# Performance work log

Measured on AMD Instinct MI355X. Metric: run time of the kernel, lower is better.

The kernel has to match this reference:

```python
import jax, jax.numpy as jnp
import numpy as np

SPEC_WINDOW = 64
SPEC_HOP = 32
PELT_PENALTY = 5.0
PATCH_MIN = 8
PATCH_MAX = 64
PATCH_GRID = 2
ANCHOR_LEN = 16
GEN_ALPHA = 1.0
GEN_BETA = 1.0
REGIME_DIM = 3

# ---------------- host-side (numpy) data-dependent segmentation ----------------

def _segment_stats(seg):
    # dominant period + normalized spectral bandwidth of a 1D segment
    n = int(seg.shape[0])
    if n < 4:
        return float(max(n, 1)), 0.0
    s = seg - seg.mean()
    spec = np.abs(np.fft.rfft(s)) ** 2
    tail = spec[1:]
    tot = float(tail.sum())
    if tot <= 0.0:
        return float(n), 0.0
    k = int(np.argmax(tail)) + 1
    dom_period = n / k
    p = tail / tot
    nf = tail.shape[0]
    f = np.arange(1, nf + 1, dtype=np.float64) / nf
    c = float((p * f).sum())
    bw = float(np.sqrt((p * (f - c) ** 2).sum()))
    return float(dom_period), bw


def _patch_length(dom_period, bw):
    raw = GEN_ALPHA * dom_period / (1.0 + GEN_BETA * bw)
    pl = int(PATCH_GRID * round(raw / PATCH_GRID))
    return int(min(max(pl, PATCH_MIN), PATCH_MAX))


def _detect_boundaries(sig):
    # local spectral features over sliding windows + PELT (L2 cost) changepoints
    L = int(sig.shape[0])
    if L <= max(2, PATCH_MIN) or L < SPEC_WINDOW:
        return [0, L]
    starts = np.arange(0, L - SPEC_WINDOW + 1, SPEC_HOP)
    frames = sig[starts[:, None] + np.arange(SPEC_WINDOW)]
    frames = frames - frames.mean(axis=1, keepdims=True)
    spec = np.abs(np.fft.rfft(frames * np.hanning(SPEC_WINDOW)[None, :], axis=1)) ** 2
    feats = np.log(spec + 1e-8)  # [n_windows, F]
    n, d = feats.shape
    cs = np.concatenate([np.zeros((1, d)), np.cumsum(feats, 0)], 0)
    cs2 = np.concatenate([np.zeros((1, d)), np.cumsum(feats ** 2, 0)], 0)
    Fc = np.full(n + 1, np.inf)
    Fc[0] = -PELT_PENALTY
    prev = np.zeros(n + 1, dtype=np.int64)
    cands = np.array([0], dtype=np.int64)
    for t in range(1, n + 1):
        nn = (t - cands).astype(np.float64)
        ssum = cs[t] - cs[cands]
        ssum2 = cs2[t] - cs2[cands]
        cost = (ssum2 - ssum ** 2 / nn[:, None]).sum(axis=1)
        vals = Fc[cands] + cost + PELT_PENALTY
        i = int(np.argmin(vals))
        Fc[t] = vals[i]
        prev[t] = cands[i]
        cands = np.concatenate([cands[vals <= Fc[t] + PELT_PENALTY], [t]])
    bps = []
    t = n
    while t > 0:
        bps.append(int(t))
        t = int(prev[t])
    bps = sorted(bps)
    bounds = [0]
    for k in bps[:-1]:
        b = int(starts[k]) if k < len(starts) else L
        b = min(b, L)
        if b - bounds[-1] >= PATCH_MIN:
            bounds.append(b)
    if L - bounds[-1] < PATCH_MIN and len(bounds) > 1:
        bounds.pop()
    bounds.append(L)
    return bounds


def _build_plan(sig):
    L = int(sig.shape[0])
    if L <= 0:
        return [(0, 0, 1, 1.0, 0.0)]
    bounds = _detect_boundaries(sig)
    plan = []
    for s, e in zip(bounds[:-1], bounds[1:]):
        if e <= s:
            continue
        dp, bw = _segment_stats(sig[s:e])
        plan.append((int(s), int(e), _patch_length(dp, bw), float(dp), float(bw)))
    if not plan:
        dp, bw = _segment_stats(sig)
        plan = [(0, L, _patch_length(dp, bw), float(dp), float(bw))]
    return plan

# ---------------- jnp ops ----------------

def _resize_linear(x, out_len):
    # matches F.interpolate(mode='linear', align_corners=False) along last axis
    in_len = x.shape[-1]
    if in_len == out_len:
        return x
    scale = in_len / out_len
    coords = (jnp.arange(out_len, dtype=jnp.float32) + 0.5) * scale - 0.5
    coords = jnp.clip(coords, 0.0, in_len - 1)
    lo = jnp.floor(coords).astype(jnp.int32)
    hi = jnp.minimum(lo + 1, in_len - 1)
    w = (coords - lo).astype(x.dtype)
    return x[..., lo] * (1 - w) + x[..., hi] * w


def setup_inputs() -> dict:
    key = jax.random.key(0)
    x = jax.random.normal(key, (32, 32, 16384), dtype=jnp.float32)
    return {"x": x}


def reference(x):
    B, C, L = x.shape
    x_np = np.asarray(x)
    plans = [_build_plan(x_np[b].mean(axis=0).astype(np.float32)) for b in range(B)]
    denom_c = float(max(L - 1, 1))
    denom_s = float(max(L, 1))

    per = []
    max_tok = 0
    for b in range(B):
        series = x[b]
        pch, sch, ech, rch = [], [], [], []
        for (s, e, pl, dp, bw) in plans[b]:
            if e <= s:
                continue
            seg_len = e - s
            regime = np.array([dp / denom_s, bw, seg_len / denom_s], dtype=np.float32)
            n_full = seg_len // pl
            full_len = n_full * pl
            if n_full > 0:
                full = jnp.transpose(series[:, s:s + full_len].reshape(C, n_full, pl), (1, 0, 2))
                pch.append(_resize_linear(full, ANCHOR_LEN))
                st = s + np.arange(n_full, dtype=np.int64) * pl
                sch.append(st)
                ech.append(st + pl)
                rch.append(np.broadcast_to(regime, (n_full, REGIME_DIM)).copy())
            if full_len < seg_len:
                pch.append(_resize_linear(series[:, s + full_len:e], ANCHOR_LEN)[None])
                sch.append(np.array([s + full_len], dtype=np.int64))
                ech.append(np.array([e], dtype=np.int64))
                rch.append(regime[None])
        patches = jnp.concatenate(pch, axis=0)
        per.append((patches, np.concatenate(sch), np.concatenate(ech), np.concatenate(rch)))
        max_tok = max(max_tok, patches.shape[0])

    pouts = []
    mask = np.zeros((B, max_tok), dtype=bool)
    start_out = np.zeros((B, max_tok), dtype=np.int32)
    end_out = np.zeros((B, max_tok), dtype=np.int32)
    center_out = np.zeros((B, max_tok, 1), dtype=np.float32)
    span_out = np.zeros((B, max_tok, 1), dtype=np.float32)
    regime_out = np.zeros((B, max_tok, REGIME_DIM), dtype=np.float32)
    n_tok = np.zeros((B,), dtype=np.int32)
    for b, (p, st, en, rg) in enumerate(per):
        n = p.shape[0]
        pouts.append(jnp.concatenate([p, jnp.zeros((max_tok - n, C, ANCHOR_LEN), x.dtype)], 0))
        mask[b, :n] = True
        start_out[b, :n] = st
        end_out[b, :n] = en
        center_out[b, :n, 0] = (st.astype(np.float32) + en.astype(np.float32) - 1.0) * 0.5 / denom_c
        span_out[b, :n, 0] = (en - st).astype(np.float32) / denom_s
        regime_out[b, :n] = rg
        n_tok[b] = n
    patches_out = jnp.stack(pouts, 0)
    return (patches_out, jnp.asarray(mask), jnp.asarray(start_out), jnp.asarray(end_out),
            jnp.asarray(center_out), jnp.asarray(span_out), jnp.asarray(regime_out), jnp.asarray(n_tok))
```

## Files before the change

### kernel.cpp

```cpp
#include <hip/hip_runtime.h>
#include <math.h>

#define Bn 32
#define Cn 32
#define Ln 16384
#define NF 511
#define NB 33
#define MAXSEG 512
#define TB 8192
#define PEN 5.0

__global__ void k_sig(const float* __restrict__ x, float* __restrict__ sig) {
    int idx = blockIdx.x * 256 + threadIdx.x;
    if (idx >= Bn * Ln) return;
    int b = idx >> 14;
    int t = idx & (Ln - 1);
    const float* p = x + ((size_t)b * Cn) * Ln + t;
    float a = p[0];
    #pragma unroll
    for (int c = 1; c < Cn; c++) a += p[(size_t)c * Ln];
    sig[idx] = a / 32.0f;
}

__global__ void k_fmean(const float* __restrict__ sig, float* __restrict__ fm) {
    int idx = blockIdx.x * 256 + threadIdx.x;
    if (idx >= Bn * NF) return;
    int b = idx / NF, f = idx - b * NF;
    const float* a = sig + b * Ln + f * 32;
    float r[8];
    #pragma unroll
    for (int j = 0; j < 8; j++) r[j] = a[j];
    #pragma unroll
    for (int base = 8; base < 64; base += 8)
        #pragma unroll
        for (int j = 0; j < 8; j++) r[j] += a[base + j];
    float res = ((r[0] + r[1]) + (r[2] + r[3])) + ((r[4] + r[5]) + (r[6] + r[7]));
    fm[idx] = res / 64.0f;
}

__global__ void k_feats(const float* __restrict__ sig, const float* __restrict__ fm,
                        double* __restrict__ feats) {
    __shared__ double v[64], ct[64], stb[64];
    int bf = blockIdx.x;
    int b = bf / NF, f = bf - b * NF;
    int i = threadIdx.x;
    double ang = (2.0 * M_PI * (double)i) / 64.0;
    double sn, cx;
    sincos(ang, &sn, &cx);
    ct[i] = cx; stb[i] = sn;
    int n2 = 2 * i - 63;
    double w = 0.5 + 0.5 * cos((M_PI * (double)n2) / 63.0);
    float m = fm[bf];
    v[i] = (double)(sig[b * Ln + f * 32 + i] - m) * w;
    __syncthreads();
    if (i < NB) {
        double re = 0.0, im = 0.0;
        for (int t = 0; t < 64; t++) {
            int j = (t * i) & 63;
            re += v[t] * ct[j];
            im += v[t] * stb[j];
        }
        double spec = re * re + im * im;
        feats[(size_t)bf * NB + i] = log(spec + 1e-8);
    }
}

__global__ void k_cumsum(const double* __restrict__ feats, double* __restrict__ cs,
                         double* __restrict__ cs2) {
    int idx = blockIdx.x * 256 + threadIdx.x;
    if (idx >= Bn * NB) return;
    int b = idx / NB, d = idx - b * NB;
    const double* fp = feats + (size_t)b * NF * NB + d;
    double* c1 = cs + (size_t)b * 512 * NB + d;
    double* c2 = cs2 + (size_t)b * 512 * NB + d;
    double a1 = 0.0, a2 = 0.0;
    c1[0] = 0.0; c2[0] = 0.0;
    for (int t = 0; t < NF; t++) {
        double vv = fp[(size_t)t * NB];
        a1 += vv;
        a2 += vv * vv;
        c1[(size_t)(t + 1) * NB] = a1;
        c2[(size_t)(t + 1) * NB] = a2;
    }
}

__global__ __launch_bounds__(256) void k_cost(const double* __restrict__ cs,
                                              const double* __restrict__ cs2,
                                              double* __restrict__ costM) {
    int z = blockIdx.x;
    int b = blockIdx.y;
    const double* c1 = cs + (size_t)b * 512 * NB;
    const double* c2 = cs2 + (size_t)b * 512 * NB;
    for (int t = z + 1; t <= NF; t += 32) {
        const double* ct1 = c1 + (size_t)t * NB;
        const double* ct2 = c2 + (size_t)t * NB;
        double* outp = costM + ((size_t)b * 512 + (size_t)t) * 512;
        for (int c = threadIdx.x; c < t; c += 256) {
            double nn = (double)(t - c);
            const double* p1 = c1 + (size_t)c * NB;
            const double* p2 = c2 + (size_t)c * NB;
            double r[8];
            #pragma unroll
            for (int j = 0; j < 8; j++) {
                double ss = ct1[j] - p1[j]; double s2 = ct2[j] - p2[j];
                r[j] = s2 - ss * ss / nn;
            }
            #pragma unroll
            for (int base = 8; base < 32; base += 8)
                #pragma unroll
                for (int j = 0; j < 8; j++) {
                    int d = base + j;
                    double ss = ct1[d] - p1[d]; double s2 = ct2[d] - p2[d];
                    r[j] += s2 - ss * ss / nn;
                }
            double res = ((r[0] + r[1]) + (r[2] + r[3])) + ((r[4] + r[5]) + (r[6] + r[7]));
            { double ss = ct1[32] - p1[32]; double s2 = ct2[32] - p2[32]; res += s2 - ss * ss / nn; }
            outp[c] = res;
        }
    }
}

template <int CTRL>
__device__ __forceinline__ double dpp_mov_f64(double v) {
    int lo = __double2loint(v), hi = __double2hiint(v);
    int slo = __builtin_amdgcn_update_dpp(lo, lo, CTRL, 0xF, 0xF, false);
    int shi = __builtin_amdgcn_update_dpp(hi, hi, CTRL, 0xF, 0xF, false);
    return __hiloint2double(shi, slo);
}
__device__ __forceinline__ double rl_f64(double v, int l) {
    int lo = __builtin_amdgcn_readlane(__double2loint(v), l);
    int hi = __builtin_amdgcn_readlane(__double2hiint(v), l);
    return __hiloint2double(hi, lo);
}
__device__ __forceinline__ double wave_min_f64(double v) {
    v = fmin(v, dpp_mov_f64<0x111>(v));
    v = fmin(v, dpp_mov_f64<0x112>(v));
    v = fmin(v, dpp_mov_f64<0x114>(v));
    v = fmin(v, dpp_mov_f64<0x118>(v));
    double a = rl_f64(v, 15), b = rl_f64(v, 31);
    double c = rl_f64(v, 47), d = rl_f64(v, 63);
    return fmin(fmin(a, b), fmin(c, d));
}

template <int NP>
__device__ __forceinline__ void pelt_step(int t, int lane, const double (&cur)[8],
                                          double (&fcreg)[8], int* __restrict__ prevOut) {
    double vals[NP];
    #pragma unroll
    for (int p = 0; p < NP; p++) vals[p] = fcreg[p] + cur[p] + PEN;
    double red[NP];
    #pragma unroll
    for (int p = 0; p < NP; p++) red[p] = vals[p];
    #pragma unroll
    for (int s = 1; s < NP; s <<= 1)
        #pragma unroll
        for (int p = 0; p + s < NP; p += 2 * s) red[p] = fmin(red[p], red[p + s]);
    double bmin = wave_min_f64(red[0]);
    int bc = 0;
    #pragma unroll
    for (int p = NP - 1; p >= 0; p--) {
        unsigned long long m = __ballot(vals[p] == bmin);
        if (m != 0ull) bc = (p << 6) + (__ffsll(m) - 1);
    }
    if (lane == 0) prevOut[t] = bc;
    double thr = bmin + PEN;
    #pragma unroll
    for (int p = 0; p < NP; p++)
        if (!(vals[p] <= thr)) fcreg[p] = INFINITY;
    #pragma unroll
    for (int p = NP - 1; p <= NP; p++)
        if (p < 8 && p == (t >> 6) && lane == (t & 63)) fcreg[p] = bmin;
}

template <int K>
__device__ __forceinline__ void pelt_phase(const double* __restrict__ cm, int lane,
                                           double (&fcreg)[8], int* __restrict__ prevOut) {
    constexpr int NP = K + 1;
    const int t0 = 64 * K + 1;
    const int t1 = (64 * K + 64 < NF) ? (64 * K + 64) : NF;
    double r0[8], r1[8], n0[8], n1[8];
    #pragma unroll
    for (int p = 0; p < NP; p++) {
        r0[p] = cm[(size_t)t0 * 512 + (p << 6) + lane];
        r1[p] = cm[(size_t)(t0 + 1) * 512 + (p << 6) + lane];
    }
    int t = t0;
    for (; t + 1 <= t1; t += 2) {
        int q0 = t + 2, q1 = t + 3;
        if (q0 > NF) q0 = NF;
        if (q1 > NF) q1 = NF;
        #pragma unroll
        for (int p = 0; p < NP; p++) {
            n0[p] = cm[(size_t)q0 * 512 + (p << 6) + lane];
            n1[p] = cm[(size_t)q1 * 512 + (p << 6) + lane];
        }
        pelt_step<NP>(t, lane, r0, fcreg, prevOut);
        pelt_step<NP>(t + 1, lane, r1, fcreg, prevOut);
        #pragma unroll
        for (int p = 0; p < NP; p++) { r0[p] = n0[p]; r1[p] = n1[p]; }
    }
    if (t <= t1) pelt_step<NP>(t, lane, r0, fcreg, prevOut);
}

__global__ __launch_bounds__(64, 1) void k_pelt(const double* __restrict__ costM,
                                                int* __restrict__ prevG) {
    int b = blockIdx.x;
    int lane = threadIdx.x;
    const double* cm = costM + (size_t)b * 512 * 512;
    int* prevOut = prevG + b * 512;
    double fcreg[8];
    #pragma unroll
    for (int p = 0; p < 8; p++) fcreg[p] = INFINITY;
    if (lane == 0) fcreg[0] = -PEN;
    pelt_phase<0>(cm, lane, fcreg, prevOut);
    pelt_phase<1>(cm, lane, fcreg, prevOut);
    pelt_phase<2>(cm, lane, fcreg, prevOut);
    pelt_phase<3>(cm, lane, fcreg, prevOut);
    pelt_phase<4>(cm, lane, fcreg, prevOut);
    pelt_phase<5>(cm, lane, fcreg, prevOut);
    pelt_phase<6>(cm, lane, fcreg, prevOut);
    pelt_phase<7>(cm, lane, fcreg, prevOut);
}

__global__ __launch_bounds__(64) void k_pelt_slow(const double* __restrict__ cs,
                                                  const double* __restrict__ cs2,
                                                  int* __restrict__ prevG) {
    __shared__ double sFc[512];
    __shared__ double sVal[512];
    __shared__ unsigned short sCand[512];
    int b = blockIdx.x;
    int lane = threadIdx.x;
    const double* c1 = cs + (size_t)b * 512 * NB;
    const double* c2 = cs2 + (size_t)b * 512 * NB;
    if (lane == 0) { sFc[0] = -PEN; sCand[0] = 0; }
    __syncthreads();
    int ncand = 1;
    for (int t = 1; t <= NF; t++) {
        const double* ct1 = c1 + (size_t)t * NB;
        const double* ct2 = c2 + (size_t)t * NB;
        int passes = (ncand + 63) >> 6;
        double bmv = INFINITY;
        int bmi = 0x7fffffff;
        for (int p = 0; p < passes; p++) {
            int slot = (p << 6) + lane;
            double val = INFINITY;
            if (slot < ncand) {
                int cc = sCand[slot];
                double nn = (double)(t - cc);
                const double* p1 = c1 + (size_t)cc * NB;
                const double* p2 = c2 + (size_t)cc * NB;
                double r[8];
                #pragma unroll
                for (int j = 0; j < 8; j++) {
                    double ss = ct1[j] - p1[j]; double s2 = ct2[j] - p2[j];
                    r[j] = s2 - ss * ss / nn;
                }
                #pragma unroll
                for (int base = 8; base < 32; base += 8)
                    #pragma unroll
                    for (int j = 0; j < 8; j++) {
                        int d = base + j;
                        double ss = ct1[d] - p1[d]; double s2 = ct2[d] - p2[d];
                        r[j] += s2 - ss * ss / nn;
                    }
                double res = ((r[0] + r[1]) + (r[2] + r[3])) + ((r[4] + r[5]) + (r[6] + r[7]));
                { double ss = ct1[32] - p1[32]; double s2 = ct2[32] - p2[32]; res += s2 - ss * ss / nn; }
                val = sFc[cc] + res + PEN;
                if (val < bmv) { bmv = val; bmi = slot; }
            }
            sVal[slot] = val;
        }
        #pragma unroll
        for (int off = 1; off < 64; off <<= 1) {
            double ov = __shfl_xor(bmv, off);
            int oi = __shfl_xor(bmi, off);
            if (ov < bmv || (ov == bmv && oi < bmi)) { bmv = ov; bmi = oi; }
        }
        double thr = bmv + PEN;
        if (lane == 0) {
            sFc[t] = bmv;
            prevG[b * 512 + t] = (int)sCand[bmi];
        }
        __syncthreads();
        int base = 0;
        for (int p = 0; p < passes; p++) {
            int slot = (p << 6) + lane;
            int cc = (slot < ncand) ? (int)sCand[slot] : 0;
            bool keep = (slot < ncand) && (sVal[slot] <= thr);
            unsigned long long mask = __ballot(keep);
            if (keep) sCand[base + __popcll(mask & ((1ull << lane) - 1ull))] = (unsigned short)cc;
            base += (int)__popcll(mask);
        }
        if (lane == 0) sCand[base] = (unsigned short)t;
        ncand = base + 1;
        __syncthreads();
    }
}

__global__ __launch_bounds__(64) void k_bounds(const int* __restrict__ prevG,
                                               int* __restrict__ segS, int* __restrict__ segE,
                                               int* __restrict__ nsegA, int* __restrict__ binoff) {
    __shared__ int sPrev[512];
    __shared__ int sBp[512];
    __shared__ int sBd[520];
    __shared__ int sNs;
    int b = blockIdx.x;
    int tid = threadIdx.x;
    const int* pv = prevG + b * 512;
    #pragma unroll
    for (int i = 0; i < 8; i++) sPrev[tid + i * 64] = pv[tid + i * 64];
    __syncthreads();
    if (tid == 0) {
        int cnt = 0, t = NF;
        while (t > 0) { sBp[cnt++] = t; t = sPrev[t]; }
        int nbv = 1; sBd[0] = 0; int last = 0;
        for (int i = cnt - 1; i >= 1; --i) {
            int k = sBp[i];
            int bb = 32 * k;
            if (bb > Ln) bb = Ln;
            if (bb - last >= 8) { sBd[nbv++] = bb; last = bb; }
        }
        if (Ln - last < 8 && nbv > 1) nbv--;
        sBd[nbv++] = Ln;
        int ns = nbv - 1;
        nsegA[b] = ns;
        sNs = ns;
    }
    __syncthreads();
    int ns = sNs;
    for (int j = tid; j < ns; j += 64) {
        int s = sBd[j], e = sBd[j + 1];
        segS[b * 512 + j] = s;
        segE[b * 512 + j] = e;
        binoff[b * 513 + j] = s >> 1;
    }
    if (tid == 0) binoff[b * 513 + ns] = sBd[ns] >> 1;
}

__global__ void k_segmean(const float* __restrict__ sig, const int* __restrict__ segS,
                          const int* __restrict__ segE, const int* __restrict__ nsegA,
                          double* __restrict__ segMean) {
    __shared__ double red[256];
    int b = blockIdx.y, j = blockIdx.x;
    if (j >= nsegA[b]) return;
    int s = segS[b * 512 + j], e = segE[b * 512 + j];
    double acc = 0.0;
    for (int i = s + threadIdx.x; i < e; i += 256) acc += (double)sig[b * Ln + i];
    red[threadIdx.x] = acc;
    __syncthreads();
    for (int st = 128; st >= 1; st >>= 1) {
        if (threadIdx.x < st) red[threadIdx.x] += red[threadIdx.x + st];
        __syncthreads();
    }
    if (threadIdx.x == 0) segMean[b * 512 + j] = red[0] / (double)(e - s);
}

__global__ __launch_bounds__(256) void k_spec(const float* __restrict__ sig,
                                              const double* __restrict__ segMean,
                                              const int* __restrict__ segS, const int* __restrict__ segE,
                                              const int* __restrict__ nsegA, const int* __restrict__ binoff,
                                              double* __restrict__ spec) {
    int b = blockIdx.y;
    int wv = threadIdx.x >> 6, lane = threadIdx.x & 63;
    int slot = blockIdx.x * 4 + wv;
    int ns = nsegA[b];
    const int* off = binoff + b * 513;
    if (slot >= off[ns]) return;
    int lo = 0, hi = ns - 1;
    while (lo < hi) { int mid = (lo + hi + 1) >> 1; if (off[mid] <= slot) lo = mid; else hi = mid - 1; }
    int j = lo;
    int s = segS[b * 512 + j], e = segE[b * 512 + j], n = e - s;
    int k = slot - off[j] + 1;
    float m32 = (float)segMean[b * 512 + j];
    long j0 = ((long)lane * (long)k) % (long)n;
    long js = (64L * (long)k) % (long)n;
    double a0 = (2.0 * M_PI * (double)j0) / (double)n;
    double as = (2.0 * M_PI * (double)js) / (double)n;
    double cr, sr, cb, sb;
    sincos(a0, &sr, &cr);
    sincos(as, &sb, &cb);
    double re = 0.0, im = 0.0;
    const float* sp = sig + b * Ln + s;
    for (int tt = lane; tt < n; tt += 64) {
        double v = (double)(sp[tt] - m32);
        re += v * cr;
        im += v * sr;
        double nc = cr * cb - sr * sb;
        sr = sr * cb + cr * sb;
        cr = nc;
    }
    #pragma unroll
    for (int o = 32; o >= 1; o >>= 1) { re += __shfl_down(re, o); im += __shfl_down(im, o); }
    if (lane == 0) spec[(size_t)b * TB + slot] = re * re + im * im;
}

__global__ void k_stats(const double* __restrict__ spec, const int* __restrict__ segS,
                        const int* __restrict__ segE, const int* __restrict__ nsegA,
                        const int* __restrict__ binoff, int* __restrict__ segPL,
                        double* __restrict__ segDP, double* __restrict__ segBW,
                        int* __restrict__ segNT) {
    __shared__ double rv[256]; __shared__ int ri[256];
    __shared__ double rt[256], rs[256];
    __shared__ double sC, sTot;
    int b = blockIdx.y, j = blockIdx.x;
    if (j >= nsegA[b]) return;
    int s = segS[b * 512 + j], e = segE[b * 512 + j], n = e - s, nf = n >> 1;
    const double* base = spec + (size_t)b * TB + binoff[b * 513 + j];
    int tid = threadIdx.x;
    double mv = -INFINITY; int mi = 0x7fffffff; double tot = 0.0, s1 = 0.0;
    for (int i = tid; i < nf; i += 256) {
        double vv = base[i];
        double f = (double)(i + 1) / (double)nf;
        tot += vv; s1 += vv * f;
        if (vv > mv) { mv = vv; mi = i; }
    }
    rv[tid] = mv; ri[tid] = mi; rt[tid] = tot; rs[tid] = s1;
    __syncthreads();
    for (int st = 128; st >= 1; st >>= 1) {
        if (tid < st) {
            double ov = rv[tid + st]; int oi = ri[tid + st];
            if (ov > rv[tid] || (ov == rv[tid] && oi < ri[tid])) { rv[tid] = ov; ri[tid] = oi; }
            rt[tid] += rt[tid + st]; rs[tid] += rs[tid + st];
        }
        __syncthreads();
    }
    if (tid == 0) { sTot = rt[0]; sC = rs[0] / rt[0]; }
    __syncthreads();
    double c = sC, totv = sTot;
    double s2 = 0.0;
    for (int i = tid; i < nf; i += 256) {
        double f = (double)(i + 1) / (double)nf;
        double d = f - c;
        s2 += base[i] * d * d;
    }
    rt[tid] = s2;
    __syncthreads();
    for (int st = 128; st >= 1; st >>= 1) {
        if (tid < st) rt[tid] += rt[tid + st];
        __syncthreads();
    }
    if (tid == 0) {
        double dp, bw;
        if (n < 4) { dp = (double)(n > 0 ? n : 1); bw = 0.0; }
        else if (!(totv > 0.0)) { dp = (double)n; bw = 0.0; }
        else { int kk = ri[0] + 1; dp = (double)n / (double)kk; bw = sqrt(rt[0] / totv); }
        double raw = 1.0 * dp / (1.0 + 1.0 * bw);
        double rr = rint(raw / 2.0);
        long pl = 2L * (long)rr;
        if (pl < 8) pl = 8;
        if (pl > 64) pl = 64;
        int nfull = n / (int)pl;
        int ntok = nfull + ((nfull * (int)pl < n) ? 1 : 0);
        segPL[b * 512 + j] = (int)pl; segDP[b * 512 + j] = dp;
        segBW[b * 512 + j] = bw; segNT[b * 512 + j] = ntok;
    }
}

__global__ __launch_bounds__(64) void k_tokpref(const int* __restrict__ nsegA,
                                                const int* __restrict__ segNT,
                                                int* __restrict__ tokoff, int* __restrict__ ntokA) {
    __shared__ int sNT[512];
    __shared__ int sOff[513];
    int b = blockIdx.x, tid = threadIdx.x;
    int ns = nsegA[b];
    for (int j = tid; j < ns; j += 64) sNT[j] = segNT[b * 512 + j];
    __syncthreads();
    if (tid == 0) {
        int off = 0;
        for (int j = 0; j < ns; j++) { sOff[j] = off; off += sNT[j]; }
        sOff[ns] = off;
        ntokA[b] = off;
    }
    __syncthreads();
    for (int j = tid; j <= ns; j += 64) tokoff[b * 513 + j] = sOff[j];
}

__global__ __launch_bounds__(256) void k_fill(const float* __restrict__ x,
                                              const int* __restrict__ segS, const int* __restrict__ segE,
                                              const int* __restrict__ segPL, const double* __restrict__ segDP,
                                              const double* __restrict__ segBW, const int* __restrict__ nsegA,
                                              const int* __restrict__ tokoff, const int* __restrict__ ntokA,
                                              float* __restrict__ out, int MT) {
    int b = blockIdx.y, tok = blockIdx.x;
    int nt = ntokA[b];
    if (tok >= nt) return;
    int ns = nsegA[b];
    const int* toff = tokoff + b * 513;
    int lo = 0, hi = ns - 1;
    while (lo < hi) { int mid = (lo + hi + 1) >> 1; if (toff[mid] <= tok) lo = mid; else hi = mid - 1; }
    int j = lo;
    int s = segS[b * 512 + j], e = segE[b * 512 + j], pl = segPL[b * 512 + j];
    int idx = tok - toff[j];
    int nfull = (e - s) / pl;
    int st, en;
    if (idx < nfull) { st = s + idx * pl; en = st + pl; }
    else { st = s + nfull * pl; en = e; }
    int ilen = en - st;
    float scale = (float)ilen / 16.0f;
    int tid = threadIdx.x;
    size_t pbase = ((size_t)(b * MT + tok)) * (Cn * 16);
    const float* xb = x + (size_t)b * Cn * Ln;
    #pragma unroll
    for (int r = 0; r < 2; r++) {
        int eidx = tid + r * 256;
        int c = eidx >> 4, jo = eidx & 15;
        float coords = ((float)jo + 0.5f) * scale - 0.5f;
        if (coords < 0.0f) coords = 0.0f;
        float mx = (float)(ilen - 1);
        if (coords > mx) coords = mx;
        int l2 = (int)floorf(coords);
        int h2 = l2 + 1;
        if (h2 > ilen - 1) h2 = ilen - 1;
        float w = coords - (float)l2;
        const float* xc = xb + (size_t)c * Ln + st;
        out[pbase + eidx] = xc[l2] * (1.0f - w) + xc[h2] * w;
    }
    if (tid == 0) {
        size_t BT = (size_t)Bn * MT;
        size_t o_mask = BT * 512;
        size_t pos = (size_t)b * MT + tok;
        out[o_mask + pos] = 1.0f;
        out[o_mask + BT + pos] = (float)st;
        out[o_mask + 2 * BT + pos] = (float)en;
        out[o_mask + 3 * BT + pos] = (((float)st + (float)en) - 1.0f) * 0.5f / 16383.0f;
        out[o_mask + 4 * BT + pos] = (float)(en - st) / 16384.0f;
        double dp = segDP[b * 512 + j], bwv = segBW[b * 512 + j];
        size_t o_rg = o_mask + 5 * BT;
        out[o_rg + pos * 3 + 0] = (float)(dp / 16384.0);
        out[o_rg + pos * 3 + 1] = (float)bwv;
        out[o_rg + pos * 3 + 2] = (float)((double)(e - s) / 16384.0);
        if (tok == 0) out[o_mask + 8 * BT + b] = (float)nt;
    }
}

extern "C" void kernel_launch(void* const* d_in, const int* in_sizes, int n_in,
                              void* d_out, int out_size, void* d_ws, size_t ws_size,
                              hipStream_t stream) {
    (void)in_sizes; (void)n_in;
    const float* x = (const float*)d_in[0];
    float* out = (float*)d_out;
    char* ws = (char*)d_ws;
    size_t o = 0;
    auto alloc = [&](size_t bytes) -> char* {
        char* r = ws + o;
        o = (o + bytes + 511) & ~(size_t)511;
        return r;
    };
    float* sig = (float*)alloc((size_t)Bn * Ln * 4);
    float* fm = (float*)alloc((size_t)Bn * NF * 4);
    double* feats = (double*)alloc((size_t)Bn * NF * NB * 8);
    double* cs = (double*)alloc((size_t)Bn * 512 * NB * 8);
    double* cs2 = (double*)alloc((size_t)Bn * 512 * NB * 8);
    int* prevG = (int*)alloc((size_t)Bn * 512 * 4);
    int* nsegA = (int*)alloc((size_t)Bn * 4);
    int* segS = (int*)alloc((size_t)Bn * 512 * 4);
    int* segE = (int*)alloc((size_t)Bn * 512 * 4);
    int* segPL = (int*)alloc((size_t)Bn * 512 * 4);
    int* segNT = (int*)alloc((size_t)Bn * 512 * 4);
    double* segDP = (double*)alloc((size_t)Bn * 512 * 8);
    double* segBW = (double*)alloc((size_t)Bn * 512 * 8);
    double* segMean = (double*)alloc((size_t)Bn * 512 * 8);
    int* binoff = (int*)alloc((size_t)Bn * 513 * 4);
    int* tokoff = (int*)alloc((size_t)Bn * 513 * 4);
    int* ntokA = (int*)alloc((size_t)Bn * 4);
    double* spec = (double*)alloc((size_t)Bn * TB * 8);
    size_t costBytes = (size_t)Bn * 512 * 512 * 8;
    double* costM = (double*)alloc(costBytes);
    bool haveCost = (o <= ws_size);

    int MT = (out_size / Bn - 1) / 520;

    hipMemsetAsync(d_out, 0, (size_t)out_size * 4, stream);
    k_sig<<<(Bn * Ln + 255) / 256, 256, 0, stream>>>(x, sig);
    k_fmean<<<(Bn * NF + 255) / 256, 256, 0, stream>>>(sig, fm);
    k_feats<<<Bn * NF, 64, 0, stream>>>(sig, fm, feats);
    k_cumsum<<<(Bn * NB + 255) / 256, 256, 0, stream>>>(feats, cs, cs2);
    if (haveCost) {
        k_cost<<<dim3(32, Bn), 256, 0, stream>>>(cs, cs2, costM);
        k_pelt<<<Bn, 64, 0, stream>>>(costM, prevG);
    } else {
        k_pelt_slow<<<Bn, 64, 0, stream>>>(cs, cs2, prevG);
    }
    k_bounds<<<Bn, 64, 0, stream>>>(prevG, segS, segE, nsegA, binoff);
    k_segmean<<<dim3(MAXSEG, Bn), 256, 0, stream>>>(sig, segS, segE, nsegA, segMean);
    k_spec<<<dim3(TB / 4, Bn), 256, 0, stream>>>(sig, segMean, segS, segE, nsegA, binoff, spec);
    k_stats<<<dim3(MAXSEG, Bn), 256, 0, stream>>>(spec, segS, segE, nsegA, binoff,
                                                  segPL, segDP, segBW, segNT);
    k_tokpref<<<Bn, 64, 0, stream>>>(nsegA, segNT, tokoff, ntokA);
    if (MT > 0)
        k_fill<<<dim3(MT, Bn), 256, 0, stream>>>(x, segS, segE, segPL, segDP, segBW,
                                                 nsegA, tokoff, ntokA, out, MT);
}
```

Before: 1.066 ms.

## Transpose cumsum layout and block cost matrix over four rows per pass

The cumulative sums are stored feature-major ([b][d][t]), so threads reading consecutive candidate indices c get coalesced loads. The cost kernel now handles four t rows per pass, staging their prefix sums in shared memory and reusing each c column load across four outputs. Rows are paired front and back (4g+1 and 508-4g) so each of the 64 blocks gets a balanced share of the triangle. The serial cumsum now writes with a stride between threads, and the fallback PELT path reads with strided gathers, so those two kernels may get slower.

```diff
diff --git a/kernel.cpp b/kernel.cpp
--- a/kernel.cpp
+++ b/kernel.cpp
@@ -65,57 +65,116 @@
     }
 }
 
-__global__ void k_cumsum(const double* __restrict__ feats, double* __restrict__ cs,
-                         double* __restrict__ cs2) {
+__global__ void k_cumsum(const double* __restrict__ feats, double* __restrict__ csT,
+                         double* __restrict__ cs2T) {
     int idx = blockIdx.x * 256 + threadIdx.x;
     if (idx >= Bn * NB) return;
     int b = idx / NB, d = idx - b * NB;
     const double* fp = feats + (size_t)b * NF * NB + d;
-    double* c1 = cs + (size_t)b * 512 * NB + d;
-    double* c2 = cs2 + (size_t)b * 512 * NB + d;
+    double* c1 = csT + ((size_t)b * NB + d) * 512;
+    double* c2 = cs2T + ((size_t)b * NB + d) * 512;
     double a1 = 0.0, a2 = 0.0;
     c1[0] = 0.0; c2[0] = 0.0;
     for (int t = 0; t < NF; t++) {
         double vv = fp[(size_t)t * NB];
         a1 += vv;
         a2 += vv * vv;
-        c1[(size_t)(t + 1) * NB] = a1;
-        c2[(size_t)(t + 1) * NB] = a2;
-    }
-}
-
-__global__ __launch_bounds__(256) void k_cost(const double* __restrict__ cs,
-                                              const double* __restrict__ cs2,
+        c1[t + 1] = a1;
+        c2[t + 1] = a2;
+    }
+}
+
+__global__ __launch_bounds__(256) void k_cost(const double* __restrict__ csT,
+                                              const double* __restrict__ cs2T,
                                               double* __restrict__ costM) {
-    int z = blockIdx.x;
+    __shared__ double s1[4][NB], s2s[4][NB];
+    int g = blockIdx.x;
     int b = blockIdx.y;
-    const double* c1 = cs + (size_t)b * 512 * NB;
-    const double* c2 = cs2 + (size_t)b * 512 * NB;
-    for (int t = z + 1; t <= NF; t += 32) {
-        const double* ct1 = c1 + (size_t)t * NB;
-        const double* ct2 = c2 + (size_t)t * NB;
-        double* outp = costM + ((size_t)b * 512 + (size_t)t) * 512;
-        for (int c = threadIdx.x; c < t; c += 256) {
-            double nn = (double)(t - c);
-            const double* p1 = c1 + (size_t)c * NB;
-            const double* p2 = c2 + (size_t)c * NB;
-            double r[8];
+    const double* c1 = csT + (size_t)b * NB * 512;
+    const double* c2 = cs2T + (size_t)b * NB * 512;
+    double* outb = costM + (size_t)b * 512 * 512;
+
+    for (int ph = 0; ph < 2; ph++) {
+        int tbase = (ph == 0) ? (4 * g + 1) : (508 - 4 * g);
+        __syncthreads();
+        for (int i = threadIdx.x; i < 4 * NB; i += 256) {
+            int ti = i / NB, j = i - ti * NB;
+            s1[ti][j]  = c1[(size_t)j * 512 + (tbase + ti)];
+            s2s[ti][j] = c2[(size_t)j * 512 + (tbase + ti)];
+        }
+        __syncthreads();
+        int t0 = tbase, t3 = tbase + 3;
+
+        for (int c = threadIdx.x; c < t0; c += 256) {
+            double nn0 = (double)(tbase     - c);
+            double nn1 = (double)(tbase + 1 - c);
+            double nn2 = (double)(tbase + 2 - c);
+            double nn3 = (double)(tbase + 3 - c);
+            double rA[8], rB[8], rC[8], rD[8];
             #pragma unroll
             for (int j = 0; j < 8; j++) {
-                double ss = ct1[j] - p1[j]; double s2 = ct2[j] - p2[j];
-                r[j] = s2 - ss * ss / nn;
+                double a1 = c1[(size_t)j * 512 + c];
+                double a2 = c2[(size_t)j * 512 + c];
+                { double ss = s1[0][j] - a1, sv = s2s[0][j] - a2; rA[j] = sv - ss * ss / nn0; }
+                { double ss = s1[1][j] - a1, sv = s2s[1][j] - a2; rB[j] = sv - ss * ss / nn1; }
+                { double ss = s1[2][j] - a1, sv = s2s[2][j] - a2; rC[j] = sv - ss * ss / nn2; }
+                { double ss = s1[3][j] - a1, sv = s2s[3][j] - a2; rD[j] = sv - ss * ss / nn3; }
             }
-            #pragma unroll
-            for (int base = 8; base < 32; base += 8)
+            for (int base = 8; base < 32; base += 8) {
                 #pragma unroll
                 for (int j = 0; j < 8; j++) {
                     int d = base + j;
-                    double ss = ct1[d] - p1[d]; double s2 = ct2[d] - p2[d];
-                    r[j] += s2 - ss * ss / nn;
+                    double a1 = c1[(size_t)d * 512 + c];
+                    double a2 = c2[(size_t)d * 512 + c];
+                    { double ss = s1[0][d] - a1, sv = s2s[0][d] - a2; rA[j] += sv - ss * ss / nn0; }
+                    { double ss = s1[1][d] - a1, sv = s2s[1][d] - a2; rB[j] += sv - ss * ss / nn1; }
+                    { double ss = s1[2][d] - a1, sv = s2s[2][d] - a2; rC[j] += sv - ss * ss / nn2; }
+                    { double ss = s1[3][d] - a1, sv = s2s[3][d] - a2; rD[j] += sv - ss * ss / nn3; }
                 }
-            double res = ((r[0] + r[1]) + (r[2] + r[3])) + ((r[4] + r[5]) + (r[6] + r[7]));
-            { double ss = ct1[32] - p1[32]; double s2 = ct2[32] - p2[32]; res += s2 - ss * ss / nn; }
-            outp[c] = res;
+            }
+            double a1 = c1[(size_t)32 * 512 + c];
+            double a2 = c2[(size_t)32 * 512 + c];
+            double res0 = ((rA[0] + rA[1]) + (rA[2] + rA[3])) + ((rA[4] + rA[5]) + (rA[6] + rA[7]));
+            double res1 = ((rB[0] + rB[1]) + (rB[2] + rB[3])) + ((rB[4] + rB[5]) + (rB[6] + rB[7]));
+            double res2 = ((rC[0] + rC[1]) + (rC[2] + rC[3])) + ((rC[4] + rC[5]) + (rC[6] + rC[7]));
+            double res3 = ((rD[0] + rD[1]) + (rD[2] + rD[3])) + ((rD[4] + rD[5]) + (rD[6] + rD[7]));
+            { double ss = s1[0][32] - a1, sv = s2s[0][32] - a2; res0 += sv - ss * ss / nn0; }
+            { double ss = s1[1][32] - a1, sv = s2s[1][32] - a2; res1 += sv - ss * ss / nn1; }
+            { double ss = s1[2][32] - a1, sv = s2s[2][32] - a2; res2 += sv - ss * ss / nn2; }
+            { double ss = s1[3][32] - a1, sv = s2s[3][32] - a2; res3 += sv - ss * ss / nn3; }
+            outb[(size_t)(tbase    ) * 512 + c] = res0;
+            outb[(size_t)(tbase + 1) * 512 + c] = res1;
+            outb[(size_t)(tbase + 2) * 512 + c] = res2;
+            outb[(size_t)(tbase + 3) * 512 + c] = res3;
+        }
+
+        for (int c = t0 + threadIdx.x; c < t3; c += 256) {
+            for (int ti = 0; ti < 4; ti++) {
+                int t = tbase + ti;
+                if (c >= t) continue;
+                double nn = (double)(t - c);
+                double r[8];
+                #pragma unroll
+                for (int j = 0; j < 8; j++) {
+                    double ss = s1[ti][j] - c1[(size_t)j * 512 + c];
+                    double sv = s2s[ti][j] - c2[(size_t)j * 512 + c];
+                    r[j] = sv - ss * ss / nn;
+                }
+                for (int base = 8; base < 32; base += 8) {
+                    #pragma unroll
+                    for (int j = 0; j < 8; j++) {
+                        int d = base + j;
+                        double ss = s1[ti][d] - c1[(size_t)d * 512 + c];
+                        double sv = s2s[ti][d] - c2[(size_t)d * 512 + c];
+                        r[j] += sv - ss * ss / nn;
+                    }
+                }
+                double res = ((r[0] + r[1]) + (r[2] + r[3])) + ((r[4] + r[5]) + (r[6] + r[7]));
+                { double ss = s1[ti][32] - c1[(size_t)32 * 512 + c];
+                  double sv = s2s[ti][32] - c2[(size_t)32 * 512 + c];
+                  res += sv - ss * ss / nn; }
+                outb[(size_t)t * 512 + c] = res;
+            }
         }
     }
 }
@@ -222,22 +281,20 @@
     pelt_phase<7>(cm, lane, fcreg, prevOut);
 }
 
-__global__ __launch_bounds__(64) void k_pelt_slow(const double* __restrict__ cs,
-                                                  const double* __restrict__ cs2,
+__global__ __launch_bounds__(64) void k_pelt_slow(const double* __restrict__ csT,
+                                                  const double* __restrict__ cs2T,
                                                   int* __restrict__ prevG) {
     __shared__ double sFc[512];
     __shared__ double sVal[512];
     __shared__ unsigned short sCand[512];
     int b = blockIdx.x;
     int lane = threadIdx.x;
-    const double* c1 = cs + (size_t)b * 512 * NB;
-    const double* c2 = cs2 + (size_t)b * 512 * NB;
+    const double* c1 = csT + (size_t)b * NB * 512;
+    const double* c2 = cs2T + (size_t)b * NB * 512;
     if (lane == 0) { sFc[0] = -PEN; sCand[0] = 0; }
     __syncthreads();
     int ncand = 1;
     for (int t = 1; t <= NF; t++) {
-        const double* ct1 = c1 + (size_t)t * NB;
-        const double* ct2 = c2 + (size_t)t * NB;
         int passes = (ncand + 63) >> 6;
         double bmv = INFINITY;
         int bmi = 0x7fffffff;
@@ -247,12 +304,11 @@
             if (slot < ncand) {
                 int cc = sCand[slot];
                 double nn = (double)(t - cc);
-                const double* p1 = c1 + (size_t)cc * NB;
-                const double* p2 = c2 + (size_t)cc * NB;
                 double r[8];
                 #pragma unroll
                 for (int j = 0; j < 8; j++) {
-                    double ss = ct1[j] - p1[j]; double s2 = ct2[j] - p2[j];
+                    double ss = c1[(size_t)j * 512 + t] - c1[(size_t)j * 512 + cc];
+                    double s2 = c2[(size_t)j * 512 + t] - c2[(size_t)j * 512 + cc];
                     r[j] = s2 - ss * ss / nn;
                 }
                 #pragma unroll
@@ -260,11 +316,14 @@
                     #pragma unroll
                     for (int j = 0; j < 8; j++) {
                         int d = base + j;
-                        double ss = ct1[d] - p1[d]; double s2 = ct2[d] - p2[d];
+                        double ss = c1[(size_t)d * 512 + t] - c1[(size_t)d * 512 + cc];
+                        double s2 = c2[(size_t)d * 512 + t] - c2[(size_t)d * 512 + cc];
                         r[j] += s2 - ss * ss / nn;
                     }
                 double res = ((r[0] + r[1]) + (r[2] + r[3])) + ((r[4] + r[5]) + (r[6] + r[7]));
-                { double ss = ct1[32] - p1[32]; double s2 = ct2[32] - p2[32]; res += s2 - ss * ss / nn; }
+                { double ss = c1[(size_t)32 * 512 + t] - c1[(size_t)32 * 512 + cc];
+                  double s2 = c2[(size_t)32 * 512 + t] - c2[(size_t)32 * 512 + cc];
+                  res += s2 - ss * ss / nn; }
                 val = sFc[cc] + res + PEN;
                 if (val < bmv) { bmv = val; bmi = slot; }
             }
@@ -549,8 +608,8 @@
     float* sig = (float*)alloc((size_t)Bn * Ln * 4);
     float* fm = (float*)alloc((size_t)Bn * NF * 4);
     double* feats = (double*)alloc((size_t)Bn * NF * NB * 8);
-    double* cs = (double*)alloc((size_t)Bn * 512 * NB * 8);
-    double* cs2 = (double*)alloc((size_t)Bn * 512 * NB * 8);
+    double* csT = (double*)alloc((size_t)Bn * NB * 512 * 8);
+    double* cs2T = (double*)alloc((size_t)Bn * NB * 512 * 8);
     int* prevG = (int*)alloc((size_t)Bn * 512 * 4);
     int* nsegA = (int*)alloc((size_t)Bn * 4);
     int* segS = (int*)alloc((size_t)Bn * 512 * 4);
@@ -574,12 +633,12 @@
     k_sig<<<(Bn * Ln + 255) / 256, 256, 0, stream>>>(x, sig);
     k_fmean<<<(Bn * NF + 255) / 256, 256, 0, stream>>>(sig, fm);
     k_feats<<<Bn * NF, 64, 0, stream>>>(sig, fm, feats);
-    k_cumsum<<<(Bn * NB + 255) / 256, 256, 0, stream>>>(feats, cs, cs2);
+    k_cumsum<<<(Bn * NB + 255) / 256, 256, 0, stream>>>(feats, csT, cs2T);
     if (haveCost) {
-        k_cost<<<dim3(32, Bn), 256, 0, stream>>>(cs, cs2, costM);
+        k_cost<<<dim3(64, Bn), 256, 0, stream>>>(csT, cs2T, costM);
         k_pelt<<<Bn, 64, 0, stream>>>(costM, prevG);
     } else {
-        k_pelt_slow<<<Bn, 64, 0, stream>>>(cs, cs2, prevG);
+        k_pelt_slow<<<Bn, 64, 0, stream>>>(csT, cs2T, prevG);
     }
     k_bounds<<<Bn, 64, 0, stream>>>(prevG, segS, segE, nsegA, binoff);
     k_segmean<<<dim3(MAXSEG, Bn), 256, 0, stream>>>(sig, segS, segE, nsegA, segMean);
```

After: 1.283 ms. 1.2x slower.
